# Optimization experiments

Measured on AMD Instinct MI355X. Metric: run time of the kernel, lower is better.

## Reference

```python
import jax, jax.numpy as jnp
import numpy as np

B, LI, LT, DM, H = 1, 2048, 384, 2560, 20
DH = DM // H  # 128
EPS = 1e-05


def _rms(x, w):
    # torch.nn.RMSNorm over last dim (inner_dim), elementwise affine w
    return x * jax.lax.rsqrt(jnp.mean(x * x, axis=-1, keepdims=True) + EPS) * w


def _apply_rope(x, rope):
    # x: [B, L, H, D]; rope: [1, L, 1, D/2, 2, 2] (flux-style freqs_cis)
    xr = x.reshape(x.shape[0], x.shape[1], x.shape[2], -1, 1, 2)  # [B,L,H,D/2,1,2]
    out = rope[..., 0] * xr[..., 0] + rope[..., 1] * xr[..., 1]   # [B,L,H,D/2,2]
    return out.reshape(x.shape)


def _sdpa(q, k, v):
    # q,k,v: [B, L, H, D] -> out [B, L, H*D]; scale 1/sqrt(D)
    scale = 1.0 / np.sqrt(q.shape[-1]).astype(np.float32)
    scores = jnp.einsum('bqhd,bkhd->bhqk', q, k) * scale
    p = jax.nn.softmax(scores, axis=-1)
    o = jnp.einsum('bhqk,bkhd->bqhd', p, v)
    return o.reshape(o.shape[0], o.shape[1], -1)


def _lin(x, W, b):
    return x @ W.T + b


def _forward(img, txt, rope, img_masks,
             Wq, bq, Wk, bk, Wv, bv, Wo, bo, qn, kn,
             Wq_t, bq_t, Wk_t, bk_t, Wv_t, bv_t, Wo_t, bo_t, qn_t, kn_t):
    bsz = img.shape[0]
    # img stream: proj -> RMSNorm -> head split
    iq = _rms(_lin(img, Wq, bq), qn).reshape(bsz, -1, H, DH)
    ik = _rms(_lin(img, Wk, bk), kn).reshape(bsz, -1, H, DH)
    iv = _lin(img, Wv, bv).reshape(bsz, -1, H, DH)
    ik = ik * img_masks[:, :, None, None]
    # txt stream
    tq = _rms(_lin(txt, Wq_t, bq_t), qn_t).reshape(bsz, -1, H, DH)
    tk = _rms(_lin(txt, Wk_t, bk_t), kn_t).reshape(bsz, -1, H, DH)
    tv = _lin(txt, Wv_t, bv_t).reshape(bsz, -1, H, DH)
    # concat streams, apply rope, attention
    q = jnp.concatenate([iq, tq], axis=1)
    k = jnp.concatenate([ik, tk], axis=1)
    v = jnp.concatenate([iv, tv], axis=1)
    q = _apply_rope(q, rope)
    k = _apply_rope(k, rope)
    attn = _sdpa(q, k, v)  # [B, LI+LT, DM]
    img_attn, txt_attn = attn[:, :LI], attn[:, LI:]
    return _lin(img_attn, Wo, bo), _lin(txt_attn, Wo_t, bo_t)


def setup_inputs() -> dict:
    key = jax.random.key(0)
    ks = jax.random.split(key, 16)
    s = 0.02
    inp = {
        'img': jax.random.normal(ks[0], (B, LI, DM), jnp.float32),
        'txt': jax.random.normal(ks[1], (B, LT, DM), jnp.float32),
        'rope': jax.random.normal(ks[2], (1, LI + LT, 1, DH // 2, 2, 2), jnp.float32),
        'img_masks': jnp.ones((B, LI), jnp.float32),
    }
    wnames = ['Wq', 'Wk', 'Wv', 'Wo', 'Wq_t', 'Wk_t', 'Wv_t', 'Wo_t']
    for i, n in enumerate(wnames):
        inp[n] = jax.random.normal(ks[3 + i], (DM, DM), jnp.float32) * s
        inp['b' + n[1:]] = jnp.zeros((DM,), jnp.float32)
    for i, n in enumerate(['qn', 'kn', 'qn_t', 'kn_t']):
        inp[n] = jax.random.uniform(ks[11 + i], (DM,), jnp.float32, 0.5, 1.5)
    return inp


def reference(img, txt, rope, img_masks,
              Wq, bq, Wk, bk, Wv, bv, Wo, bo, qn, kn,
              Wq_t, bq_t, Wk_t, bk_t, Wv_t, bv_t, Wo_t, bo_t, qn_t, kn_t):
    return _forward(img, txt, rope, img_masks,
                    Wq, bq, Wk, bk, Wv, bv, Wo, bo, qn, kn,
                    Wq_t, bq_t, Wk_t, bk_t, Wv_t, bv_t, Wo_t, bo_t, qn_t, kn_t)
```

## Files before the change

### kernel.cpp

```cpp
#include <hip/hip_runtime.h>
#include <math.h>

#define LI 2048
#define LT 384
#define LSEQ 2432
#define DM 2560
#define NH 20
#define DH 128
#define SCALE 0.08838834764831845f

typedef __bf16 bf16x8 __attribute__((ext_vector_type(8)));
typedef __bf16 bf16x4 __attribute__((ext_vector_type(4)));
typedef __bf16 bf16x2 __attribute__((ext_vector_type(2)));
typedef float f32x4 __attribute__((ext_vector_type(4)));

__device__ __forceinline__ void async_copy16(const void* gsrc, void* lds_uniform) {
    __builtin_amdgcn_global_load_lds(
        (const __attribute__((address_space(1))) unsigned int*)gsrc,
        (__attribute__((address_space(3))) unsigned int*)lds_uniform,
        16, 0, 0);
}


__global__ __launch_bounds__(256) void cvt8_kernel(
    const float* __restrict__ s0, const float* __restrict__ s1,
    const float* __restrict__ s2, const float* __restrict__ s3,
    const float* __restrict__ s4, const float* __restrict__ s5,
    const float* __restrict__ s6, const float* __restrict__ s7,
    __bf16* __restrict__ dst)
{
    const float* srcs[8] = {s0, s1, s2, s3, s4, s5, s6, s7};
    const float* s = srcs[blockIdx.y];
    __bf16* d = dst + (size_t)blockIdx.y * (size_t)DM * DM;
    int i = blockIdx.x * 256 + threadIdx.x;
    const float4* sp = (const float4*)s + (size_t)i * 2;
    float4 a = sp[0], b = sp[1];
    bf16x8 o = {(__bf16)a.x, (__bf16)a.y, (__bf16)a.z, (__bf16)a.w,
                (__bf16)b.x, (__bf16)b.y, (__bf16)b.z, (__bf16)b.w};
    *((bf16x8*)d + i) = o;
}

__global__ __launch_bounds__(256) void cvt_kernel(
    const float* __restrict__ s, __bf16* __restrict__ d, int n8)
{
    int i = blockIdx.x * 256 + threadIdx.x;
    if (i >= n8) return;
    const float4* sp = (const float4*)s + (size_t)i * 2;
    float4 a = sp[0], b = sp[1];
    bf16x8 o = {(__bf16)a.x, (__bf16)a.y, (__bf16)a.z, (__bf16)a.w,
                (__bf16)b.x, (__bf16)b.y, (__bf16)b.z, (__bf16)b.w};
    *((bf16x8*)d + i) = o;
}


__device__ __forceinline__ void gemm_core(
    const __bf16* __restrict__ Ab,
    const __bf16* __restrict__ Bb,
    const float* __restrict__ bias,
    float* __restrict__ Cb,
    __bf16* sA, __bf16* sB)
{
    const int t = threadIdx.x, wave = t >> 6, lane = t & 63;
    const int l15 = lane & 15, quad = lane >> 4;
    const int wm = wave >> 1, wn = wave & 1;

    f32x4 acc[4][4];
#pragma unroll
    for (int i = 0; i < 4; i++)
#pragma unroll
        for (int j = 0; j < 4; j++) acc[i][j] = f32x4{0.f, 0.f, 0.f, 0.f};

    size_t soff[4];
#pragma unroll
    for (int j = 0; j < 4; j++) {
        int c = j * 256 + t;
        int row = c >> 3, u = c & 7;
        soff[j] = (size_t)row * DM + ((u ^ (row & 7)) * 8);
    }

    for (int k0 = 0; k0 < DM; k0 += 64) {
        __syncthreads();
#pragma unroll
        for (int j = 0; j < 4; j++)
            async_copy16(Ab + soff[j] + k0, (char*)sA + (j * 256 + wave * 64) * 16);
#pragma unroll
        for (int j = 0; j < 4; j++)
            async_copy16(Bb + soff[j] + k0, (char*)sB + (j * 256 + wave * 64) * 16);
        __syncthreads();

#pragma unroll
        for (int ks = 0; ks < 2; ks++) {
            bf16x8 af[4], bg[4];
#pragma unroll
            for (int mt = 0; mt < 4; mt++) {
                int r = wm * 64 + mt * 16 + l15;
                af[mt] = *(const bf16x8*)(sA + r * 64 + (((quad + ks * 4) ^ (r & 7)) * 8));
            }
#pragma unroll
            for (int nt = 0; nt < 4; nt++) {
                int r = wn * 64 + nt * 16 + l15;
                bg[nt] = *(const bf16x8*)(sB + r * 64 + (((quad + ks * 4) ^ (r & 7)) * 8));
            }
#pragma unroll
            for (int mt = 0; mt < 4; mt++)
#pragma unroll
                for (int nt = 0; nt < 4; nt++)
                    acc[mt][nt] = __builtin_amdgcn_mfma_f32_16x16x32_bf16(af[mt], bg[nt], acc[mt][nt], 0, 0, 0);
        }
    }

#pragma unroll
    for (int mt = 0; mt < 4; mt++) {
        const int row = wm * 64 + mt * 16 + quad * 4;
#pragma unroll
        for (int nt = 0; nt < 4; nt++) {
            const int col = wn * 64 + nt * 16 + l15;
            const float bv = bias[col];
            float* cp = Cb + (size_t)row * DM + col;
            cp[0]        = acc[mt][nt][0] + bv;
            cp[DM]       = acc[mt][nt][1] + bv;
            cp[2 * DM]   = acc[mt][nt][2] + bv;
            cp[3 * DM]   = acc[mt][nt][3] + bv;
        }
    }
}

__global__ __launch_bounds__(256, 4) void gemm_qkv_kernel(
    const __bf16* __restrict__ xbf, const __bf16* __restrict__ wbf,
    const float* __restrict__ bq, const float* __restrict__ bk, const float* __restrict__ bv,
    const float* __restrict__ bq_t, const float* __restrict__ bk_t, const float* __restrict__ bv_t,
    float* __restrict__ qraw, float* __restrict__ kraw, float* __restrict__ vraw)
{
    __shared__ alignas(16) __bf16 sA[128 * 64];
    __shared__ alignas(16) __bf16 sB[128 * 64];
    const int nblk = blockIdx.x, mblk = blockIdx.y;
    const int which = nblk / 20;
    const int nloc = (nblk % 20) * 128;
    const bool is_txt = (mblk >= 16);
    const size_t WELEM = (size_t)DM * DM;
    const int widx = which + (is_txt ? 4 : 0);
    const __bf16* W = wbf + (size_t)widx * WELEM;
    const float* bias = (which == 0) ? (is_txt ? bq_t : bq)
                      : (which == 1) ? (is_txt ? bk_t : bk)
                                     : (is_txt ? bv_t : bv);
    float* C = (which == 0) ? qraw : (which == 1) ? kraw : vraw;
    gemm_core(xbf + (size_t)mblk * 128 * DM, W + (size_t)nloc * DM, bias + nloc,
              C + (size_t)mblk * 128 * DM + nloc, sA, sB);
}

__global__ __launch_bounds__(256, 4) void gemm_out_kernel(
    const __bf16* __restrict__ attnbf, const __bf16* __restrict__ wbf,
    const float* __restrict__ bo, const float* __restrict__ bo_t,
    float* __restrict__ out)
{
    __shared__ alignas(16) __bf16 sA[128 * 64];
    __shared__ alignas(16) __bf16 sB[128 * 64];
    const int nblk = blockIdx.x, mblk = blockIdx.y;
    const bool is_txt = (mblk >= 16);
    const size_t WELEM = (size_t)DM * DM;
    const __bf16* W = wbf + (size_t)(is_txt ? 7 : 3) * WELEM;
    const float* bias = (is_txt ? bo_t : bo) + nblk * 128;
    gemm_core(attnbf + (size_t)mblk * 128 * DM, W + (size_t)nblk * 128 * DM, bias,
              out + (size_t)mblk * 128 * DM + nblk * 128, sA, sB);
}


__global__ __launch_bounds__(256) void rmsrope_kernel(
    const float* __restrict__ qraw, const float* __restrict__ kraw,
    const float* __restrict__ rope, const float* __restrict__ img_masks,
    const float* __restrict__ qn, const float* __restrict__ kn,
    const float* __restrict__ qn_t, const float* __restrict__ kn_t,
    __bf16* __restrict__ qbf, __bf16* __restrict__ kbf)
{
    const int l = blockIdx.x, t = threadIdx.x;
    const int wave = t >> 6, lane = t & 63;
    const bool is_img = (l < LI);
    const float* qw = is_img ? qn : qn_t;
    const float* kw = is_img ? kn : kn_t;
    const float kmask = is_img ? img_masks[l] : 1.0f;
    const float* qr = qraw + (size_t)l * DM;
    const float* kr = kraw + (size_t)l * DM;

    float2 qv[5], kv[5];
    float sq = 0.f, sk = 0.f;
#pragma unroll
    for (int j = 0; j < 5; j++) {
        int c2 = j * 256 + t;
        qv[j] = *(const float2*)(qr + 2 * c2);
        kv[j] = *(const float2*)(kr + 2 * c2);
        sq += qv[j].x * qv[j].x + qv[j].y * qv[j].y;
        sk += kv[j].x * kv[j].x + kv[j].y * kv[j].y;
    }
#pragma unroll
    for (int m = 32; m; m >>= 1) { sq += __shfl_xor(sq, m); sk += __shfl_xor(sk, m); }
    __shared__ float redq[4], redk[4];
    if (lane == 0) { redq[wave] = sq; redk[wave] = sk; }
    __syncthreads();
    sq = redq[0] + redq[1] + redq[2] + redq[3];
    sk = redk[0] + redk[1] + redk[2] + redk[3];
    const float rq = rsqrtf(sq * (1.0f / DM) + 1e-5f);
    const float rk = rsqrtf(sk * (1.0f / DM) + 1e-5f) * kmask;

#pragma unroll
    for (int j = 0; j < 5; j++) {
        int c2 = j * 256 + t;
        int c = 2 * c2;
        float4 rp = *(const float4*)(rope + ((size_t)l * 64 + (c2 & 63)) * 4);
        float2 w2q = *(const float2*)(qw + c);
        float2 w2k = *(const float2*)(kw + c);
        float x0 = qv[j].x * rq * w2q.x, x1 = qv[j].y * rq * w2q.y;
        bf16x2 oq = {(__bf16)(rp.x * x0 + rp.y * x1), (__bf16)(rp.z * x0 + rp.w * x1)};
        *(bf16x2*)(qbf + (size_t)l * DM + c) = oq;
        float y0 = kv[j].x * rk * w2k.x, y1 = kv[j].y * rk * w2k.y;
        bf16x2 ok = {(__bf16)(rp.x * y0 + rp.y * y1), (__bf16)(rp.z * y0 + rp.w * y1)};
        *(bf16x2*)(kbf + (size_t)l * DM + c) = ok;
    }
}


__global__ __launch_bounds__(256) void transpose_cvt_kernel(
    const float* __restrict__ src, __bf16* __restrict__ dst)
{
    __shared__ float tile[32][33];
    const int c0 = blockIdx.x * 32;
    const int r0 = blockIdx.y * 32;
    const int tc = threadIdx.x & 31, tr = threadIdx.x >> 5;
#pragma unroll
    for (int j = 0; j < 4; j++)
        tile[tr + j * 8][tc] = src[(size_t)(r0 + tr + j * 8) * DM + c0 + tc];
    __syncthreads();
#pragma unroll
    for (int j = 0; j < 4; j++)
        dst[(size_t)(c0 + tr + j * 8) * LSEQ + r0 + tc] = (__bf16)tile[tc][tr + j * 8];
}


__global__ __launch_bounds__(256, 4) void flash_kernel(
    const __bf16* __restrict__ qb, const __bf16* __restrict__ kb,
    const __bf16* __restrict__ vt, __bf16* __restrict__ ob)
{
    __shared__ alignas(16) __bf16 sK[64 * DH];
    __shared__ alignas(16) __bf16 sV[DH * 64];
    __shared__ alignas(16) __bf16 sP[4 * 16 * 64];
    const int head = blockIdx.x;
    const int q0 = blockIdx.y * 64;
    const int t = threadIdx.x, wave = t >> 6, lane = t & 63;
    const int l15 = lane & 15, quad = lane >> 4;
    const int qrow = q0 + wave * 16 + l15;

    bf16x8 aq[4];
#pragma unroll
    for (int d = 0; d < 4; d++)
        aq[d] = *(const bf16x8*)(qb + (size_t)qrow * DM + head * DH + d * 32 + quad * 8);

    size_t koff[4], voff[4];
#pragma unroll
    for (int j = 0; j < 4; j++) {
        int ck = (wave * 4 + j) * 64 + lane;
        int krow = ck >> 4, ku = (ck & 15) ^ (krow & 7);
        koff[j] = (size_t)krow * DM + head * DH + ku * 8;
        int cv = (wave * 4 + j) * 64 + lane;
        int vrow = cv >> 3, vu = (cv & 7) ^ (vrow & 7);
        voff[j] = (size_t)(head * DH + vrow) * LSEQ + vu * 8;
    }

    f32x4 o[8];
#pragma unroll
    for (int i = 0; i < 8; i++) o[i] = f32x4{0.f, 0.f, 0.f, 0.f};
    float m_i = -INFINITY, l_i = 0.f;
    __bf16* pw = sP + wave * (16 * 64);

    for (int kv0 = 0; kv0 < LSEQ; kv0 += 64) {
        __syncthreads();
#pragma unroll
        for (int j = 0; j < 4; j++)
            async_copy16(kb + koff[j] + (size_t)kv0 * DM, (char*)sK + (wave * 4 + j) * 1024);
#pragma unroll
        for (int j = 0; j < 4; j++)
            async_copy16(vt + voff[j] + kv0, (char*)sV + (wave * 4 + j) * 1024);
        __syncthreads();

        f32x4 st[4];
#pragma unroll
        for (int b = 0; b < 4; b++) {
            st[b] = f32x4{0.f, 0.f, 0.f, 0.f};
#pragma unroll
            for (int d = 0; d < 4; d++) {
                int row = b * 16 + l15;
                bf16x8 ak = *(const bf16x8*)(sK + row * 128 + (((d * 4 + quad) ^ (row & 7)) * 8));
                st[b] = __builtin_amdgcn_mfma_f32_16x16x32_bf16(ak, aq[d], st[b], 0, 0, 0);
            }
        }

        float mx = m_i;
#pragma unroll
        for (int b = 0; b < 4; b++)
#pragma unroll
            for (int r = 0; r < 4; r++) { st[b][r] *= SCALE; mx = fmaxf(mx, st[b][r]); }
        mx = fmaxf(mx, __shfl_xor(mx, 16));
        mx = fmaxf(mx, __shfl_xor(mx, 32));
        const float al = __expf(m_i - mx);
        m_i = mx;
        float sum = 0.f;
#pragma unroll
        for (int b = 0; b < 4; b++)
#pragma unroll
            for (int r = 0; r < 4; r++) {
                float p = __expf(st[b][r] - mx);
                st[b][r] = p;
                sum += p;
            }
        sum += __shfl_xor(sum, 16);
        sum += __shfl_xor(sum, 32);
        l_i = l_i * al + sum;

#pragma unroll
        for (int b = 0; b < 4; b++) {
            bf16x4 pk = {(__bf16)st[b][0], (__bf16)st[b][1], (__bf16)st[b][2], (__bf16)st[b][3]};
            int u = 2 * b + (quad >> 1);
            *(bf16x4*)(pw + l15 * 64 + ((u ^ (l15 & 7)) * 8) + (quad & 1) * 4) = pk;
        }

        float alr[4];
#pragma unroll
        for (int r = 0; r < 4; r++) alr[r] = __shfl(al, quad * 4 + r);
#pragma unroll
        for (int i = 0; i < 8; i++) {
            f32x4 tmp = o[i];
            tmp[0] *= alr[0]; tmp[1] *= alr[1]; tmp[2] *= alr[2]; tmp[3] *= alr[3];
            o[i] = tmp;
        }
        __asm__ volatile("s_waitcnt lgkmcnt(0)" ::: "memory");

        bf16x8 ap0 = *(const bf16x8*)(pw + l15 * 64 + ((quad ^ (l15 & 7)) * 8));
        bf16x8 ap1 = *(const bf16x8*)(pw + l15 * 64 + (((4 + quad) ^ (l15 & 7)) * 8));
#pragma unroll
        for (int n2 = 0; n2 < 8; n2++) {
            int row = n2 * 16 + l15;
            bf16x8 bv0 = *(const bf16x8*)(sV + row * 64 + ((quad ^ (row & 7)) * 8));
            bf16x8 bv1 = *(const bf16x8*)(sV + row * 64 + (((4 + quad) ^ (row & 7)) * 8));
            o[n2] = __builtin_amdgcn_mfma_f32_16x16x32_bf16(ap0, bv0, o[n2], 0, 0, 0);
            o[n2] = __builtin_amdgcn_mfma_f32_16x16x32_bf16(ap1, bv1, o[n2], 0, 0, 0);
        }
    }

    const float inv = 1.0f / l_i;
    float invr[4];
#pragma unroll
    for (int r = 0; r < 4; r++) invr[r] = __shfl(inv, quad * 4 + r);
#pragma unroll
    for (int n2 = 0; n2 < 8; n2++)
#pragma unroll
        for (int r = 0; r < 4; r++)
            ob[(size_t)(q0 + wave * 16 + quad * 4 + r) * DM + head * DH + n2 * 16 + l15] =
                (__bf16)(o[n2][r] * invr[r]);
}


extern "C" void kernel_launch(void* const* d_in, const int* in_sizes, int n_in,
                              void* d_out, int out_size, void* d_ws, size_t ws_size,
                              hipStream_t stream) {
    const float* img       = (const float*)d_in[0];
    const float* txt       = (const float*)d_in[1];
    const float* rope      = (const float*)d_in[2];
    const float* img_masks = (const float*)d_in[3];
    const float* Wq   = (const float*)d_in[4];  const float* bq   = (const float*)d_in[5];
    const float* Wk   = (const float*)d_in[6];  const float* bk   = (const float*)d_in[7];
    const float* Wv   = (const float*)d_in[8];  const float* bv   = (const float*)d_in[9];
    const float* Wo   = (const float*)d_in[10]; const float* bo   = (const float*)d_in[11];
    const float* Wq_t = (const float*)d_in[12]; const float* bq_t = (const float*)d_in[13];
    const float* Wk_t = (const float*)d_in[14]; const float* bk_t = (const float*)d_in[15];
    const float* Wv_t = (const float*)d_in[16]; const float* bv_t = (const float*)d_in[17];
    const float* Wo_t = (const float*)d_in[18]; const float* bo_t = (const float*)d_in[19];
    const float* qn   = (const float*)d_in[20]; const float* kn   = (const float*)d_in[21];
    const float* qn_t = (const float*)d_in[22]; const float* kn_t = (const float*)d_in[23];
    float* out = (float*)d_out;

    const size_t WELEM = (size_t)DM * DM;
    const size_t XELEM = (size_t)LSEQ * DM;

    __bf16* wbf  = (__bf16*)d_ws;
    __bf16* xbf  = wbf + 8 * WELEM;
    float*  qraw = (float*)(xbf + XELEM);
    float*  kraw = qraw + XELEM;
    float*  vraw = kraw + XELEM;
    __bf16* qbf  = (__bf16*)(vraw + XELEM);
    __bf16* kbf  = qbf + XELEM;
    __bf16* vt   = kbf + XELEM;
    __bf16* attnbf = (__bf16*)qraw;

    cvt8_kernel<<<dim3((int)(WELEM / 8 / 256), 8), 256, 0, stream>>>(
        Wq, Wk, Wv, Wo, Wq_t, Wk_t, Wv_t, Wo_t, wbf);
    cvt_kernel<<<dim3((LI * DM / 8 + 255) / 256), 256, 0, stream>>>(img, xbf, LI * DM / 8);
    cvt_kernel<<<dim3((LT * DM / 8 + 255) / 256), 256, 0, stream>>>(
        txt, xbf + (size_t)LI * DM, LT * DM / 8);

    gemm_qkv_kernel<<<dim3(60, 19), 256, 0, stream>>>(
        xbf, wbf, bq, bk, bv, bq_t, bk_t, bv_t, qraw, kraw, vraw);

    rmsrope_kernel<<<dim3(LSEQ), 256, 0, stream>>>(
        qraw, kraw, rope, img_masks, qn, kn, qn_t, kn_t, qbf, kbf);

    transpose_cvt_kernel<<<dim3(DM / 32, LSEQ / 32), 256, 0, stream>>>(vraw, vt);

    flash_kernel<<<dim3(NH, LSEQ / 64), 256, 0, stream>>>(qbf, kbf, vt, attnbf);

    gemm_out_kernel<<<dim3(20, 19), 256, 0, stream>>>(attnbf, wbf, bo, bo_t, out);
}
```

Measured before the change: 573.7 us.

## Replace QKV GEMM with 256x256-tile 8-wave double-buffered pipelined kernel

Swaps the 128x128-tile QKV projection GEMM for a 512-thread kernel. Each block computes a 256x256 tile using 128KB of dynamic LDS, double-buffered with async global-to-LDS copies. The inner loop is split into four MFMA phases separated by barriers. The next K-slice prefetch is interleaved between phases, and s_setprio is raised around the MFMA bursts. The aim is more operand reuse per LDS load and better overlap of loads with matrix math. The last M block overlaps the previous txt block so the 2432 rows fit in 256-row tiles, which means some rows are computed twice. The flash attention MFMA loops also get setprio hints.

```diff
diff --git a/kernel.cpp b/kernel.cpp
--- a/kernel.cpp
+++ b/kernel.cpp
@@ -7,6 +7,7 @@
 #define DM 2560
 #define NH 20
 #define DH 128
+#define NT_K 40
 #define SCALE 0.08838834764831845f
 
 typedef __bf16 bf16x8 __attribute__((ext_vector_type(8)));
@@ -20,6 +21,10 @@
         (__attribute__((address_space(3))) unsigned int*)lds_uniform,
         16, 0, 0);
 }
+
+#define SBAR()  __builtin_amdgcn_s_barrier()
+#define LGKM0() asm volatile("s_waitcnt lgkmcnt(0)" ::: "memory")
+#define CFENCE() asm volatile("" ::: "memory")
 
 
 __global__ __launch_bounds__(256) void cvt8_kernel(
@@ -125,29 +130,6 @@
     }
 }
 
-__global__ __launch_bounds__(256, 4) void gemm_qkv_kernel(
-    const __bf16* __restrict__ xbf, const __bf16* __restrict__ wbf,
-    const float* __restrict__ bq, const float* __restrict__ bk, const float* __restrict__ bv,
-    const float* __restrict__ bq_t, const float* __restrict__ bk_t, const float* __restrict__ bv_t,
-    float* __restrict__ qraw, float* __restrict__ kraw, float* __restrict__ vraw)
-{
-    __shared__ alignas(16) __bf16 sA[128 * 64];
-    __shared__ alignas(16) __bf16 sB[128 * 64];
-    const int nblk = blockIdx.x, mblk = blockIdx.y;
-    const int which = nblk / 20;
-    const int nloc = (nblk % 20) * 128;
-    const bool is_txt = (mblk >= 16);
-    const size_t WELEM = (size_t)DM * DM;
-    const int widx = which + (is_txt ? 4 : 0);
-    const __bf16* W = wbf + (size_t)widx * WELEM;
-    const float* bias = (which == 0) ? (is_txt ? bq_t : bq)
-                      : (which == 1) ? (is_txt ? bk_t : bk)
-                                     : (is_txt ? bv_t : bv);
-    float* C = (which == 0) ? qraw : (which == 1) ? kraw : vraw;
-    gemm_core(xbf + (size_t)mblk * 128 * DM, W + (size_t)nloc * DM, bias + nloc,
-              C + (size_t)mblk * 128 * DM + nloc, sA, sB);
-}
-
 __global__ __launch_bounds__(256, 4) void gemm_out_kernel(
     const __bf16* __restrict__ attnbf, const __bf16* __restrict__ wbf,
     const float* __restrict__ bo, const float* __restrict__ bo_t,
@@ -162,6 +144,179 @@
     const float* bias = (is_txt ? bo_t : bo) + nblk * 128;
     gemm_core(attnbf + (size_t)mblk * 128 * DM, W + (size_t)nblk * 128 * DM, bias,
               out + (size_t)mblk * 128 * DM + nblk * 128, sA, sB);
+}
+
+
+__device__ __forceinline__ void stage_half2(
+    const __bf16* panel, char* dst, int k0, size_t soff0, size_t soff1)
+{
+    async_copy16(panel + soff0 + k0, dst);
+    async_copy16(panel + soff1 + k0, dst + 8192);
+    async_copy16(panel + (size_t)128 * DM + soff0 + k0, dst + 16384);
+    async_copy16(panel + (size_t)128 * DM + soff1 + k0, dst + 16384 + 8192);
+}
+
+__device__ __forceinline__ void gemm8_core(
+    const __bf16* __restrict__ Ap,
+    const __bf16* __restrict__ Bp,
+    const float* __restrict__ bias,
+    float* __restrict__ Cb,
+    __bf16* sA, __bf16* sB)
+{
+    const int t = threadIdx.x;
+    const int wave = t >> 6, lane = t & 63;
+    const int l15 = lane & 15, quad = lane >> 4;
+    const int wm = wave >> 2, wn = wave & 3;
+    const int sw = l15 & 7;
+
+    const int srow = t >> 3;
+    const size_t soff0 = (size_t)srow * DM + (((t & 7) ^ (srow & 7)) * 8);
+    const size_t soff1 = soff0 + (size_t)64 * DM;
+
+    char* const dA = (char*)sA + wave * 1024;
+    char* const dB = (char*)sB + wave * 1024;
+
+    f32x4 acc[8][4];
+#pragma unroll
+    for (int i = 0; i < 8; i++)
+#pragma unroll
+        for (int j = 0; j < 4; j++) acc[i][j] = f32x4{0.f, 0.f, 0.f, 0.f};
+
+    stage_half2(Ap, dA, 0, soff0, soff1);
+    stage_half2(Bp, dB, 0, soff0, soff1);
+    CFENCE();
+    stage_half2(Ap, dA + 32768, 64, soff0, soff1);
+    stage_half2(Bp, dB + 32768, 64, soff0, soff1);
+    asm volatile("s_waitcnt vmcnt(8)" ::: "memory");
+    SBAR();
+
+    for (int tau = 0; tau < NT_K; ++tau) {
+        const __bf16* bA = sA + ((tau & 1) << 14);
+        const __bf16* bB = sB + ((tau & 1) << 14);
+        char* dAc = dA + ((tau & 1) << 15);
+        char* dBc = dB + ((tau & 1) << 15);
+        const int kpf = tau * 64 + 128;
+        const bool pf = (kpf < DM);
+
+        const __bf16* rA = bA + (size_t)(wm * 128 + l15) * 64;
+        const __bf16* rB = bB + (size_t)(wn * 64 + l15) * 64;
+
+        bf16x8 a0[4][2], b0[2][2], b1[2][2];
+
+#pragma unroll
+        for (int mt = 0; mt < 4; mt++)
+#pragma unroll
+            for (int ks = 0; ks < 2; ks++)
+                a0[mt][ks] = *(const bf16x8*)(rA + mt * (16 * 64) + (((ks * 4 + quad) ^ sw) * 8));
+#pragma unroll
+        for (int nt = 0; nt < 2; nt++)
+#pragma unroll
+            for (int ks = 0; ks < 2; ks++)
+                b0[nt][ks] = *(const bf16x8*)(rB + nt * (16 * 64) + (((ks * 4 + quad) ^ sw) * 8));
+        SBAR(); LGKM0();
+        __builtin_amdgcn_s_setprio(1);
+#pragma unroll
+        for (int ks = 0; ks < 2; ks++)
+#pragma unroll
+            for (int mt = 0; mt < 4; mt++)
+#pragma unroll
+                for (int nt = 0; nt < 2; nt++)
+                    acc[mt][nt] = __builtin_amdgcn_mfma_f32_16x16x32_bf16(a0[mt][ks], b0[nt][ks], acc[mt][nt], 0, 0, 0);
+        __builtin_amdgcn_s_setprio(0);
+        SBAR();
+
+#pragma unroll
+        for (int nt = 0; nt < 2; nt++)
+#pragma unroll
+            for (int ks = 0; ks < 2; ks++)
+                b1[nt][ks] = *(const bf16x8*)(rB + (nt + 2) * (16 * 64) + (((ks * 4 + quad) ^ sw) * 8));
+        SBAR(); LGKM0();
+        __builtin_amdgcn_s_setprio(1);
+#pragma unroll
+        for (int ks = 0; ks < 2; ks++)
+#pragma unroll
+            for (int mt = 0; mt < 4; mt++)
+#pragma unroll
+                for (int nt = 0; nt < 2; nt++)
+                    acc[mt][nt + 2] = __builtin_amdgcn_mfma_f32_16x16x32_bf16(a0[mt][ks], b1[nt][ks], acc[mt][nt + 2], 0, 0, 0);
+        __builtin_amdgcn_s_setprio(0);
+        SBAR();
+
+#pragma unroll
+        for (int mt = 0; mt < 4; mt++)
+#pragma unroll
+            for (int ks = 0; ks < 2; ks++)
+                a0[mt][ks] = *(const bf16x8*)(rA + (mt + 4) * (16 * 64) + (((ks * 4 + quad) ^ sw) * 8));
+        if (pf) stage_half2(Bp, dBc, kpf, soff0, soff1);
+        SBAR(); LGKM0();
+        __builtin_amdgcn_s_setprio(1);
+#pragma unroll
+        for (int ks = 0; ks < 2; ks++)
+#pragma unroll
+            for (int mt = 0; mt < 4; mt++)
+#pragma unroll
+                for (int nt = 0; nt < 2; nt++)
+                    acc[mt + 4][nt] = __builtin_amdgcn_mfma_f32_16x16x32_bf16(a0[mt][ks], b0[nt][ks], acc[mt + 4][nt], 0, 0, 0);
+        __builtin_amdgcn_s_setprio(0);
+        SBAR();
+
+        if (pf) stage_half2(Ap, dAc, kpf, soff0, soff1);
+        SBAR();
+        __builtin_amdgcn_s_setprio(1);
+#pragma unroll
+        for (int ks = 0; ks < 2; ks++)
+#pragma unroll
+            for (int mt = 0; mt < 4; mt++)
+#pragma unroll
+                for (int nt = 0; nt < 2; nt++)
+                    acc[mt + 4][nt + 2] = __builtin_amdgcn_mfma_f32_16x16x32_bf16(a0[mt][ks], b1[nt][ks], acc[mt + 4][nt + 2], 0, 0, 0);
+        __builtin_amdgcn_s_setprio(0);
+        if (tau == NT_K - 2) { asm volatile("s_waitcnt vmcnt(0)" ::: "memory"); }
+        else                 { asm volatile("s_waitcnt vmcnt(8)" ::: "memory"); }
+        SBAR();
+    }
+
+    float bvl[4];
+#pragma unroll
+    for (int nt = 0; nt < 4; nt++) bvl[nt] = bias[wn * 64 + nt * 16 + l15];
+#pragma unroll
+    for (int mt = 0; mt < 8; mt++) {
+        const int row = wm * 128 + mt * 16 + quad * 4;
+#pragma unroll
+        for (int nt = 0; nt < 4; nt++) {
+            float* cp = Cb + (size_t)row * DM + wn * 64 + nt * 16 + l15;
+            cp[0]      = acc[mt][nt][0] + bvl[nt];
+            cp[DM]     = acc[mt][nt][1] + bvl[nt];
+            cp[2 * DM] = acc[mt][nt][2] + bvl[nt];
+            cp[3 * DM] = acc[mt][nt][3] + bvl[nt];
+        }
+    }
+}
+
+__global__ __launch_bounds__(512, 2) void gemm8_qkv_kernel(
+    const __bf16* __restrict__ xbf, const __bf16* __restrict__ wbf,
+    const float* __restrict__ bq, const float* __restrict__ bk, const float* __restrict__ bv,
+    const float* __restrict__ bq_t, const float* __restrict__ bk_t, const float* __restrict__ bv_t,
+    float* __restrict__ qraw, float* __restrict__ kraw, float* __restrict__ vraw)
+{
+    extern __shared__ __align__(16) char dynsmem[];
+    __bf16* sA = (__bf16*)dynsmem;
+    __bf16* sB = (__bf16*)(dynsmem + 65536);
+
+    const int nblk = blockIdx.x, mblk = blockIdx.y;
+    const int which = nblk / 10;
+    const int nloc = (nblk % 10) * 256;
+    const int mstart = (mblk < 9) ? (mblk * 256) : (LSEQ - 256);
+    const bool is_txt = (mblk >= 8);
+    const size_t WELEM = (size_t)DM * DM;
+    const int widx = which + (is_txt ? 4 : 0);
+    const __bf16* W = wbf + (size_t)widx * WELEM;
+    const float* bias = (which == 0) ? (is_txt ? bq_t : bq)
+                      : (which == 1) ? (is_txt ? bk_t : bk)
+                                     : (is_txt ? bv_t : bv);
+    float* C = (which == 0) ? qraw : (which == 1) ? kraw : vraw;
+    gemm8_core(xbf + (size_t)mstart * DM, W + (size_t)nloc * DM, bias + nloc,
+               C + (size_t)mstart * DM + nloc, sA, sB);
 }
 
 
@@ -281,6 +436,7 @@
         __syncthreads();
 
         f32x4 st[4];
+        __builtin_amdgcn_s_setprio(1);
 #pragma unroll
         for (int b = 0; b < 4; b++) {
             st[b] = f32x4{0.f, 0.f, 0.f, 0.f};
@@ -291,6 +447,7 @@
                 st[b] = __builtin_amdgcn_mfma_f32_16x16x32_bf16(ak, aq[d], st[b], 0, 0, 0);
             }
         }
+        __builtin_amdgcn_s_setprio(0);
 
         float mx = m_i;
 #pragma unroll
@@ -334,6 +491,7 @@
 
         bf16x8 ap0 = *(const bf16x8*)(pw + l15 * 64 + ((quad ^ (l15 & 7)) * 8));
         bf16x8 ap1 = *(const bf16x8*)(pw + l15 * 64 + (((4 + quad) ^ (l15 & 7)) * 8));
+        __builtin_amdgcn_s_setprio(1);
 #pragma unroll
         for (int n2 = 0; n2 < 8; n2++) {
             int row = n2 * 16 + l15;
@@ -342,6 +500,7 @@
             o[n2] = __builtin_amdgcn_mfma_f32_16x16x32_bf16(ap0, bv0, o[n2], 0, 0, 0);
             o[n2] = __builtin_amdgcn_mfma_f32_16x16x32_bf16(ap1, bv1, o[n2], 0, 0, 0);
         }
+        __builtin_amdgcn_s_setprio(0);
     }
 
     const float inv = 1.0f / l_i;
@@ -376,6 +535,13 @@
     const float* qn_t = (const float*)d_in[22]; const float* kn_t = (const float*)d_in[23];
     float* out = (float*)d_out;
 
+    static bool inited = false;
+    if (!inited) {
+        hipFuncSetAttribute(reinterpret_cast<const void*>(gemm8_qkv_kernel),
+                            hipFuncAttributeMaxDynamicSharedMemorySize, 131072);
+        inited = true;
+    }
+
     const size_t WELEM = (size_t)DM * DM;
     const size_t XELEM = (size_t)LSEQ * DM;
 
@@ -395,7 +561,7 @@
     cvt_kernel<<<dim3((LT * DM / 8 + 255) / 256), 256, 0, stream>>>(
         txt, xbf + (size_t)LI * DM, LT * DM / 8);
 
-    gemm_qkv_kernel<<<dim3(60, 19), 256, 0, stream>>>(
+    gemm8_qkv_kernel<<<dim3(30, 10), 512, 131072, stream>>>(
         xbf, wbf, bq, bk, bv, bq_t, bk_t, bv_t, qraw, kraw, vraw);
 
     rmsrope_kernel<<<dim3(LSEQ), 256, 0, stream>>>(
```

Measured after the change: 607.0 us. +5.8%, slower.

## Register-prefetch next K/V tile in flash attention, split QKV GEMM launch

Applied to the files above, without the earlier changes.

The flash kernel drops the direct global-to-LDS async copies. It now loads the next K/V tile into registers while the current tile is computed, then stores those registers to LDS at the start of the next iteration, which overlaps global latency with MFMA work. Wave priority is raised around the MFMA sections and offsets become 32-bit ints. The QKV GEMM launch is also split into two kernels over row blocks, which adds a launch and may change scheduling. The extra registers could lower occupancy.

```diff
diff --git a/kernel.cpp b/kernel.cpp
--- a/kernel.cpp
+++ b/kernel.cpp
@@ -125,15 +125,14 @@
     }
 }
 
-__global__ __launch_bounds__(256, 4) void gemm_qkv_kernel(
+__device__ __forceinline__ void qkv_body(
+    int nblk, int mblk,
     const __bf16* __restrict__ xbf, const __bf16* __restrict__ wbf,
     const float* __restrict__ bq, const float* __restrict__ bk, const float* __restrict__ bv,
     const float* __restrict__ bq_t, const float* __restrict__ bk_t, const float* __restrict__ bv_t,
-    float* __restrict__ qraw, float* __restrict__ kraw, float* __restrict__ vraw)
-{
-    __shared__ alignas(16) __bf16 sA[128 * 64];
-    __shared__ alignas(16) __bf16 sB[128 * 64];
-    const int nblk = blockIdx.x, mblk = blockIdx.y;
+    float* __restrict__ qraw, float* __restrict__ kraw, float* __restrict__ vraw,
+    __bf16* sA, __bf16* sB)
+{
     const int which = nblk / 20;
     const int nloc = (nblk % 20) * 128;
     const bool is_txt = (mblk >= 16);
@@ -148,6 +147,30 @@
               C + (size_t)mblk * 128 * DM + nloc, sA, sB);
 }
 
+__global__ __launch_bounds__(256, 4) void gemm_qkv_a_kernel(
+    const __bf16* __restrict__ xbf, const __bf16* __restrict__ wbf,
+    const float* __restrict__ bq, const float* __restrict__ bk, const float* __restrict__ bv,
+    const float* __restrict__ bq_t, const float* __restrict__ bk_t, const float* __restrict__ bv_t,
+    float* __restrict__ qraw, float* __restrict__ kraw, float* __restrict__ vraw)
+{
+    __shared__ alignas(16) __bf16 sA[128 * 64];
+    __shared__ alignas(16) __bf16 sB[128 * 64];
+    qkv_body(blockIdx.x, blockIdx.y, xbf, wbf, bq, bk, bv, bq_t, bk_t, bv_t,
+             qraw, kraw, vraw, sA, sB);
+}
+
+__global__ __launch_bounds__(256, 4) void gemm_qkv_b_kernel(
+    const __bf16* __restrict__ xbf, const __bf16* __restrict__ wbf,
+    const float* __restrict__ bq, const float* __restrict__ bk, const float* __restrict__ bv,
+    const float* __restrict__ bq_t, const float* __restrict__ bk_t, const float* __restrict__ bv_t,
+    float* __restrict__ qraw, float* __restrict__ kraw, float* __restrict__ vraw)
+{
+    __shared__ alignas(16) __bf16 sA[128 * 64];
+    __shared__ alignas(16) __bf16 sB[128 * 64];
+    qkv_body(blockIdx.x, blockIdx.y + 10, xbf, wbf, bq, bk, bv, bq_t, bk_t, bv_t,
+             qraw, kraw, vraw, sA, sB);
+}
+
 __global__ __launch_bounds__(256, 4) void gemm_out_kernel(
     const __bf16* __restrict__ attnbf, const __bf16* __restrict__ wbf,
     const float* __restrict__ bo, const float* __restrict__ bo_t,
@@ -253,16 +276,18 @@
     for (int d = 0; d < 4; d++)
         aq[d] = *(const bf16x8*)(qb + (size_t)qrow * DM + head * DH + d * 32 + quad * 8);
 
-    size_t koff[4], voff[4];
+    int koff[4], voff[4];
 #pragma unroll
     for (int j = 0; j < 4; j++) {
         int ck = (wave * 4 + j) * 64 + lane;
         int krow = ck >> 4, ku = (ck & 15) ^ (krow & 7);
-        koff[j] = (size_t)krow * DM + head * DH + ku * 8;
+        koff[j] = krow * DM + head * DH + ku * 8;
         int cv = (wave * 4 + j) * 64 + lane;
         int vrow = cv >> 3, vu = (cv & 7) ^ (vrow & 7);
-        voff[j] = (size_t)(head * DH + vrow) * LSEQ + vu * 8;
-    }
+        voff[j] = (head * DH + vrow) * LSEQ + vu * 8;
+    }
+    char* const dK = (char*)sK + wave * 4096 + lane * 16;
+    char* const dV = (char*)sV + wave * 4096 + lane * 16;
 
     f32x4 o[8];
 #pragma unroll
@@ -270,17 +295,32 @@
     float m_i = -INFINITY, l_i = 0.f;
     __bf16* pw = sP + wave * (16 * 64);
 
+    bf16x8 rk[4], rv[4];
+#pragma unroll
+    for (int j = 0; j < 4; j++) {
+        rk[j] = *(const bf16x8*)(kb + koff[j]);
+        rv[j] = *(const bf16x8*)(vt + voff[j]);
+    }
+
     for (int kv0 = 0; kv0 < LSEQ; kv0 += 64) {
         __syncthreads();
 #pragma unroll
-        for (int j = 0; j < 4; j++)
-            async_copy16(kb + koff[j] + (size_t)kv0 * DM, (char*)sK + (wave * 4 + j) * 1024);
-#pragma unroll
-        for (int j = 0; j < 4; j++)
-            async_copy16(vt + voff[j] + kv0, (char*)sV + (wave * 4 + j) * 1024);
+        for (int j = 0; j < 4; j++) {
+            *(bf16x8*)(dK + j * 1024) = rk[j];
+            *(bf16x8*)(dV + j * 1024) = rv[j];
+        }
         __syncthreads();
 
+        if (kv0 + 64 < LSEQ) {
+#pragma unroll
+            for (int j = 0; j < 4; j++) {
+                rk[j] = *(const bf16x8*)(kb + koff[j] + (size_t)(kv0 + 64) * DM);
+                rv[j] = *(const bf16x8*)(vt + voff[j] + (kv0 + 64));
+            }
+        }
+
         f32x4 st[4];
+        __builtin_amdgcn_s_setprio(1);
 #pragma unroll
         for (int b = 0; b < 4; b++) {
             st[b] = f32x4{0.f, 0.f, 0.f, 0.f};
@@ -291,6 +331,7 @@
                 st[b] = __builtin_amdgcn_mfma_f32_16x16x32_bf16(ak, aq[d], st[b], 0, 0, 0);
             }
         }
+        __builtin_amdgcn_s_setprio(0);
 
         float mx = m_i;
 #pragma unroll
@@ -334,6 +375,7 @@
 
         bf16x8 ap0 = *(const bf16x8*)(pw + l15 * 64 + ((quad ^ (l15 & 7)) * 8));
         bf16x8 ap1 = *(const bf16x8*)(pw + l15 * 64 + (((4 + quad) ^ (l15 & 7)) * 8));
+        __builtin_amdgcn_s_setprio(1);
 #pragma unroll
         for (int n2 = 0; n2 < 8; n2++) {
             int row = n2 * 16 + l15;
@@ -342,6 +384,7 @@
             o[n2] = __builtin_amdgcn_mfma_f32_16x16x32_bf16(ap0, bv0, o[n2], 0, 0, 0);
             o[n2] = __builtin_amdgcn_mfma_f32_16x16x32_bf16(ap1, bv1, o[n2], 0, 0, 0);
         }
+        __builtin_amdgcn_s_setprio(0);
     }
 
     const float inv = 1.0f / l_i;
@@ -395,7 +438,9 @@
     cvt_kernel<<<dim3((LT * DM / 8 + 255) / 256), 256, 0, stream>>>(
         txt, xbf + (size_t)LI * DM, LT * DM / 8);
 
-    gemm_qkv_kernel<<<dim3(60, 19), 256, 0, stream>>>(
+    gemm_qkv_a_kernel<<<dim3(60, 10), 256, 0, stream>>>(
+        xbf, wbf, bq, bk, bv, bq_t, bk_t, bv_t, qraw, kraw, vraw);
+    gemm_qkv_b_kernel<<<dim3(60, 9), 256, 0, stream>>>(
         xbf, wbf, bq, bk, bv, bq_t, bk_t, bv_t, qraw, kraw, vraw);
 
     rmsrope_kernel<<<dim3(LSEQ), 256, 0, stream>>>(
```

After: 612.1 us. +6.7%, slower.
